# Performance work log

Hardware: AMD Instinct MI355X
Metric: run time of the kernel (lower is better)

The kernel has to match this reference:

```python
import jax, jax.numpy as jnp
import numpy as np

B, S, W = 64, 256, 16
V, CV = 50000, 100
E, CD, H, T = 256, 64, 512, 50


def lstm_scan(xs, wih, whh, bih, bhh, reverse=False):
    # xs: [T, N, D]; PyTorch LSTMCell gate order i, f, g, o
    Hh = whh.shape[1]
    def step(carry, x):
        h, c = carry
        g = x @ wih.T + bih + h @ whh.T + bhh
        i, f, gg, o = jnp.split(g, 4, axis=-1)
        c = jax.nn.sigmoid(f) * c + jax.nn.sigmoid(i) * jnp.tanh(gg)
        h = jax.nn.sigmoid(o) * jnp.tanh(c)
        return (h, c), h
    z = jnp.zeros((xs.shape[1], Hh), xs.dtype)
    (hT, _), hs = jax.lax.scan(step, (z, z), xs, reverse=reverse)
    return hT, hs


def setup_inputs():
    key = jax.random.key(0)
    ki = iter(jax.random.split(key, 64))
    def p(shape):
        return (jax.random.normal(next(ki), shape) * 0.05).astype(jnp.float32)
    def cell(din, h):
        return p((4 * h, din)), p((4 * h, h)), p((4 * h,)), p((4 * h,))
    inp = {
        'sentence': jax.random.randint(next(ki), (B, S), 0, V),
        'char_sentence': jax.random.randint(next(ki), (B, S, W), 0, CV),
        'w_emb': p((V, E)),
        'w_char': p((CV, CD)),
    }
    for name, din, h in [('cf', CD, E // 2), ('cb', CD, E // 2),
                         ('l1f', E, H), ('l1b', E, H),
                         ('l2f', 2 * H, H), ('l2b', 2 * H, H)]:
        wih, whh, bih, bhh = cell(din, h)
        inp[name + '_wih'] = wih; inp[name + '_whh'] = whh
        inp[name + '_bih'] = bih; inp[name + '_bhh'] = bhh
    inp['w_final'] = p((E, 2 * E)); inp['b_final'] = p((E,))
    inp['w_tag'] = p((T, 2 * H)); inp['b_tag'] = p((T,))
    return inp


def reference(sentence, char_sentence, w_emb, w_char,
              cf_wih, cf_whh, cf_bih, cf_bhh,
              cb_wih, cb_whh, cb_bih, cb_bhh,
              l1f_wih, l1f_whh, l1f_bih, l1f_bhh,
              l1b_wih, l1b_whh, l1b_bih, l1b_bhh,
              l2f_wih, l2f_whh, l2f_bih, l2f_bhh,
              l2b_wih, l2b_whh, l2b_bih, l2b_bhh,
              w_final, b_final, w_tag, b_tag):
    w_char = w_char.at[0].set(0.0)            # padding_idx=0
    word_emb = w_emb[sentence]                # [B,S,E]
    ce = w_char[char_sentence]                # [B,S,W,CD]
    b, s, w, cd = ce.shape
    ce = ce.reshape(b * s, w, cd).transpose(1, 0, 2)   # [W, B*S, CD]
    hf, _ = lstm_scan(ce, cf_wih, cf_whh, cf_bih, cf_bhh)
    hb, _ = lstm_scan(ce, cb_wih, cb_whh, cb_bih, cb_bhh, reverse=True)
    char_word = jnp.concatenate([hf, hb], -1).reshape(b, s, -1)  # [B,S,E]
    embeds = jnp.concatenate([word_emb, char_word], -1) @ w_final.T + b_final
    xs = embeds.transpose(1, 0, 2)            # [S,B,E]
    _, o1f = lstm_scan(xs, l1f_wih, l1f_whh, l1f_bih, l1f_bhh)
    _, o1b = lstm_scan(xs, l1b_wih, l1b_whh, l1b_bih, l1b_bhh, reverse=True)
    o1 = jnp.concatenate([o1f, o1b], -1)      # [S,B,2H]
    _, o2f = lstm_scan(o1, l2f_wih, l2f_whh, l2f_bih, l2f_bhh)
    _, o2b = lstm_scan(o1, l2b_wih, l2b_whh, l2b_bih, l2b_bhh, reverse=True)
    o2 = jnp.concatenate([o2f, o2b], -1).transpose(1, 0, 2)  # [B,S,2H]
    # dropout is identity in eval mode
    return o2 @ w_tag.T + b_tag               # [B,S,T]
```

## Files before the change

kernel.cpp:

```cpp
#include <hip/hip_runtime.h>

typedef unsigned short u16;
typedef unsigned long long ull;
typedef short short8 __attribute__((ext_vector_type(8)));
typedef float float4_ __attribute__((ext_vector_type(4)));
typedef short8 short8a __attribute__((may_alias));
typedef float4_ float4a __attribute__((may_alias));
typedef ull ulla __attribute__((may_alias));

#define MFMA16(a, b, c) __builtin_amdgcn_mfma_f32_16x16x32_bf16((a), (b), (c), 0, 0, 0)

static __device__ __forceinline__ float b2f(u16 v) { return __uint_as_float(((unsigned)v) << 16); }
static __device__ __forceinline__ u16 f2b(float f) {
  unsigned x = __float_as_uint(f);
  return (u16)((x + 0x7fffu + ((x >> 16) & 1u)) >> 16);
}
static __device__ __forceinline__ float ldv(const void* p, long long i, int isbf) {
  return isbf ? b2f(((const u16*)p)[i]) : ((const float*)p)[i];
}
static __device__ __forceinline__ float sigm(float x) { return 1.f / (1.f + __expf(-x)); }
static __device__ __forceinline__ float tanh_(float x) { return 1.f - 2.f / (__expf(2.f * x) + 1.f); }
static __device__ __forceinline__ float4_ splat4(float v) { float4_ r; r[0]=v; r[1]=v; r[2]=v; r[3]=v; return r; }

__global__ __launch_bounds__(256) void k_detect(const unsigned* __restrict__ wtag, int* __restrict__ flag) {
  __shared__ int cs;
  if (threadIdx.x == 0) cs = 0;
  __syncthreads();
  int hits = 0;
  for (int i = threadIdx.x; i < 1024; i += 256) {
    unsigned b = (wtag[i] >> 8) & 0x7fu;
    hits += (b >= 0x36u && b <= 0x3fu) ? 1 : 0;
  }
  atomicAdd(&cs, hits);
  __syncthreads();
  if (threadIdx.x == 0) *flag = (cs > 512) ? 1 : 0;
}

struct WSegs { const void* src[15]; int dst[15]; int n[15]; };
__global__ __launch_bounds__(256) void k_convw(WSegs s, u16* __restrict__ wt, const int* __restrict__ flagp) {
  const int isbf = *flagp;
  const long long total8 = 9830400 / 8;
  for (long long i8 = (long long)blockIdx.x * 256 + threadIdx.x; i8 < total8; i8 += (long long)gridDim.x * 256) {
    const long long i = i8 * 8;
    int k = 0;
#pragma unroll
    for (int j = 1; j < 15; ++j) if (i >= (long long)s.dst[j]) k = j;
    const long long loc = i - s.dst[k];
    short8 out;
    if (!s.src[k]) {
      for (int j = 0; j < 8; ++j) out[j] = 0;
    } else if (isbf) {
      out = *(const short8a*)((const u16*)s.src[k] + loc);
    } else {
      const float* fp = (const float*)s.src[k] + loc;
      const float4_ f0 = *(const float4a*)fp;
      const float4_ f1 = *(const float4a*)(fp + 4);
#pragma unroll
      for (int j = 0; j < 4; ++j) { out[j] = (short)f2b(f0[j]); out[j + 4] = (short)f2b(f1[j]); }
    }
    *(short8a*)(wt + i) = out;
  }
}

struct BSegs { const void* a[8]; const void* b[8]; int dst[8]; int n[8]; int np[8]; };
__global__ __launch_bounds__(256) void k_convb(BSegs s, float* __restrict__ bias, const int* __restrict__ flagp) {
  const int isbf = *flagp;
  for (int i = blockIdx.x * 256 + threadIdx.x; i < 9536; i += gridDim.x * 256) {
    int k = 0;
#pragma unroll
    for (int j = 1; j < 8; ++j) if (i >= s.dst[j]) k = j;
    const int loc = i - s.dst[k];
    float v = 0.f;
    if (loc < s.n[k]) {
      v = ldv(s.a[k], loc, isbf);
      if (s.b[k]) v += ldv(s.b[k], loc, isbf);
    }
    bias[i] = v;
  }
}

__global__ __launch_bounds__(128) void k_wordgather(const int* __restrict__ sent, const void* __restrict__ wemb,
                                                    u16* __restrict__ cat, const int* __restrict__ flagp) {
  const int n = blockIdx.x;
  const int idx = sent[n];
  const int isbf = *flagp;
  for (int d = threadIdx.x; d < 256; d += 128)
    cat[(long long)n * 512 + d] = f2b(ldv(wemb, (long long)idx * 256 + d, isbf));
}

__global__ __launch_bounds__(256) void k_char(const int* __restrict__ cs, const void* __restrict__ wchar,
                                              const u16* __restrict__ wihF, const u16* __restrict__ whhF,
                                              const u16* __restrict__ wihB, const u16* __restrict__ whhB,
                                              const float* __restrict__ biasF, const float* __restrict__ biasB,
                                              u16* __restrict__ cat, const int* __restrict__ flagp) {
  const int dir = blockIdx.y;
  const int nb = blockIdx.x;
  const u16* wih = dir ? wihB : wihF;
  const u16* whh = dir ? whhB : whhF;
  const float* bias = dir ? biasB : biasF;
  const int isbf = *flagp;
  __shared__ __align__(16) u16 xs[64][72];
  __shared__ __align__(16) u16 hs[64][136];
  const int tid = threadIdx.x, wv = tid >> 6, lane = tid & 63;
  for (int i = tid; i < 64 * 136; i += 256) ((u16*)hs)[i] = 0;
  float c[2][4][4];
#pragma unroll
  for (int a1 = 0; a1 < 2; ++a1)
#pragma unroll
    for (int a2 = 0; a2 < 4; ++a2)
#pragma unroll
      for (int a3 = 0; a3 < 4; ++a3) c[a1][a2][a3] = 0.f;

  for (int tt = 0; tt < 16; ++tt) {
    const int t = dir ? (15 - tt) : tt;
    {
      const int sid = tid >> 2, part = tid & 3;
      const int n = nb * 64 + sid;
      const int idx = cs[n * 16 + t];
#pragma unroll
      for (int q = 0; q < 16; ++q) {
        const int d2 = part * 16 + q;
        float v = 0.f;
        if (idx != 0) v = ldv(wchar, (long long)idx * 64 + d2, isbf);
        xs[sid][d2] = f2b(v);
      }
    }
    __syncthreads();
    float4_ acc[2][4][4];
#pragma unroll
    for (int ut = 0; ut < 2; ++ut)
#pragma unroll
      for (int g = 0; g < 4; ++g) {
        const float bv = bias[g * 128 + (wv + 4 * ut) * 16 + (lane & 15)];
#pragma unroll
        for (int rt = 0; rt < 4; ++rt) acc[ut][g][rt] = splat4(bv);
      }
#pragma unroll
    for (int kc = 0; kc < 6; ++kc) {
      short8 a[4];
      if (kc < 2) {
#pragma unroll
        for (int rt = 0; rt < 4; ++rt)
          a[rt] = *(const short8a*)&xs[rt * 16 + (lane & 15)][kc * 32 + (lane >> 4) * 8];
      } else {
#pragma unroll
        for (int rt = 0; rt < 4; ++rt)
          a[rt] = *(const short8a*)&hs[rt * 16 + (lane & 15)][(kc - 2) * 32 + (lane >> 4) * 8];
      }
#pragma unroll
      for (int ut = 0; ut < 2; ++ut)
#pragma unroll
        for (int g = 0; g < 4; ++g) {
          const int col = g * 128 + (wv + 4 * ut) * 16 + (lane & 15);
          short8 bfr;
          if (kc < 2) bfr = *(const short8a*)(wih + col * 64 + kc * 32 + (lane >> 4) * 8);
          else        bfr = *(const short8a*)(whh + col * 128 + (kc - 2) * 32 + (lane >> 4) * 8);
#pragma unroll
          for (int rt = 0; rt < 4; ++rt) acc[ut][g][rt] = MFMA16(a[rt], bfr, acc[ut][g][rt]);
        }
    }
    __syncthreads();
#pragma unroll
    for (int ut = 0; ut < 2; ++ut)
#pragma unroll
      for (int rt = 0; rt < 4; ++rt)
#pragma unroll
        for (int r = 0; r < 4; ++r) {
          const float iv = acc[ut][0][rt][r];
          const float fv = acc[ut][1][rt][r];
          const float gv = acc[ut][2][rt][r];
          const float ov = acc[ut][3][rt][r];
          float& cc = c[ut][rt][r];
          cc = sigm(fv) * cc + sigm(iv) * tanh_(gv);
          const float h = sigm(ov) * tanh_(cc);
          const int seq = rt * 16 + (lane >> 4) * 4 + r;
          const int u = (wv + 4 * ut) * 16 + (lane & 15);
          const u16 hv = f2b(h);
          hs[seq][u] = hv;
          if (tt == 15) cat[(long long)(nb * 64 + seq) * 512 + 256 + dir * 128 + u] = hv;
        }
  }
}

template <int TM, int TN, int PERM, int OUTM>
__global__ __launch_bounds__(256) void k_gemm(const u16* __restrict__ A, const u16* __restrict__ Wt,
                                              const float* __restrict__ bias, void* __restrict__ Cout,
                                              const int N, const int K, const int ldc,
                                              const int* __restrict__ flagp) {
  constexpr int RT = TM / 16;
  constexpr int CPW = TN / 64;
  const int bm = blockIdx.x, bn = blockIdx.y;
  const int tid = threadIdx.x, wv = tid >> 6, lane = tid & 63;
  __shared__ __align__(16) u16 As[TM][72];
  float4_ acc[CPW][RT];
#pragma unroll
  for (int ci = 0; ci < CPW; ++ci)
#pragma unroll
    for (int rt = 0; rt < RT; ++rt) acc[ci][rt] = splat4(0.f);
  const int nk = K >> 6;
  for (int kc = 0; kc < nk; ++kc) {
    __syncthreads();
    for (int idx = tid; idx < TM * 4; idx += 256) {
      const int r = idx >> 2, sg = idx & 3;
      const u16* src = A + (long long)(bm * TM + r) * K + kc * 64 + sg * 16;
      *(short8a*)&As[r][sg * 16] = *(const short8a*)src;
      *(short8a*)&As[r][sg * 16 + 8] = *(const short8a*)(src + 8);
    }
    __syncthreads();
#pragma unroll
    for (int kk = 0; kk < 2; ++kk) {
      short8 af[RT];
#pragma unroll
      for (int rt = 0; rt < RT; ++rt)
        af[rt] = *(const short8a*)&As[rt * 16 + (lane & 15)][kk * 32 + (lane >> 4) * 8];
#pragma unroll
      for (int ci = 0; ci < CPW; ++ci) {
        const int ct = wv + ci * 4;
        const short8 bf = *(const short8a*)(Wt + (long long)(bn * TN + ct * 16 + (lane & 15)) * K +
                                            kc * 64 + kk * 32 + (lane >> 4) * 8);
#pragma unroll
        for (int rt = 0; rt < RT; ++rt) acc[ci][rt] = MFMA16(af[rt], bf, acc[ci][rt]);
      }
    }
  }
  const int isbf = (OUTM == 1) ? *flagp : 0;
#pragma unroll
  for (int ci = 0; ci < CPW; ++ci)
#pragma unroll
    for (int rt = 0; rt < RT; ++rt)
#pragma unroll
      for (int r = 0; r < 4; ++r) {
        const int row = bm * TM + rt * 16 + (lane >> 4) * 4 + r;
        const int col = bn * TN + (wv + ci * 4) * 16 + (lane & 15);
        if (col < N) {
          const float v = acc[ci][rt][r] + bias[col];
          long long orow;
          if (PERM == 0) orow = row;
          else if (PERM == 1) orow = (long long)(row & 255) * 64 + (row >> 8);
          else orow = (long long)(row & 63) * 256 + (row >> 6);
          if (OUTM == 0) ((u16*)Cout)[orow * ldc + col] = f2b(v);
          else if (isbf) ((u16*)Cout)[orow * ldc + col] = f2b(v);
          else ((float*)Cout)[orow * ldc + col] = v;
        }
      }
}

__global__ __launch_bounds__(512, 1) void k_scan(const u16* __restrict__ pre0, const u16* __restrict__ pre1,
                                                 const u16* __restrict__ whh0, const u16* __restrict__ whh1,
                                                 u16* __restrict__ o_out, const u16* __restrict__ zbuf,
                                                 int* __restrict__ flags) {
  const int dir = blockIdx.y, blk = blockIdx.x;
  const u16* __restrict__ pre = dir ? pre1 : pre0;
  const u16* __restrict__ whh = dir ? whh1 : whh0;
  int* myflags = flags + dir * 512;
  const int u0 = blk * 32;
  __shared__ __align__(16) u16 hstage[64 * 512];
  __shared__ __align__(16) float xch[8 * 64 * 32];
  const int tid = threadIdx.x, lane = tid & 63;
  const int wv = tid >> 6;
  const int l15 = lane & 15, q = lane >> 4;
  const int g = wv & 3, kh = wv >> 2;

  float4_ swf[2][8];
#pragma unroll
  for (int ci = 0; ci < 2; ++ci)
#pragma unroll
    for (int kc = 0; kc < 8; ++kc)
      swf[ci][kc] = *(const float4a*)(whh + (long long)(g * 512 + u0 + ci * 16 + l15) * 512 +
                                      kh * 256 + kc * 32 + q * 8);

  const int bb = tid >> 3;
  const int t8 = tid & 7;
  float c4[4];
#pragma unroll
  for (int j = 0; j < 4; ++j) c4[j] = 0.f;

  ull pr[4], prn[4];
  {
    const int t0 = dir ? 255 : 0;
    const u16* pb = pre + (long long)(t0 * 64 + bb) * 2048 + u0 + t8 * 4;
#pragma unroll
    for (int g2 = 0; g2 < 4; ++g2) pr[g2] = *(const ulla*)(pb + g2 * 512);
  }

  for (int tt = 0; tt < 256; ++tt) {
    const int t = dir ? (255 - tt) : tt;

    {
      const u16* base;
      if (tt == 0) {
        base = zbuf + dir * 512;
      } else {
        const int tp = dir ? (t + 1) : (t - 1);
        base = o_out + (long long)tp * 65536 + dir * 512;
      }
      const int off = lane * 8;
#pragma unroll
      for (int it = 0; it < 8; ++it) {
        const int row = wv + it * 8;
        const float4_ v = *(const float4a*)(base + (long long)row * 1024 + off);
        *(float4a*)((char*)hstage + row * 1024 + ((off * 2) ^ ((row & 7) << 4))) = v;
      }
    }
    __syncthreads();

    float4_ acc[2][4];
#pragma unroll
    for (int ci = 0; ci < 2; ++ci)
#pragma unroll
      for (int bt = 0; bt < 4; ++bt) acc[ci][bt] = splat4(0.f);
    const char* hsb = (const char*)hstage;
#pragma unroll
    for (int kc = 0; kc < 8; ++kc) {
      const short8 w0 = __builtin_bit_cast(short8, swf[0][kc]);
      const short8 w1 = __builtin_bit_cast(short8, swf[1][kc]);
#pragma unroll
      for (int bt = 0; bt < 4; ++bt) {
        const int row = bt * 16 + l15;
        const short8 A = *(const short8a*)(hsb + row * 1024 +
                          ((kh * 512 + kc * 64 + q * 16) ^ ((row & 7) << 4)));
        acc[0][bt] = MFMA16(w0, A, acc[0][bt]);
        acc[1][bt] = MFMA16(w1, A, acc[1][bt]);
      }
    }

#pragma unroll
    for (int ci = 0; ci < 2; ++ci)
#pragma unroll
      for (int bt = 0; bt < 4; ++bt) {
        const int b = bt * 16 + l15;
        *(float4a*)&xch[(((kh * 4 + g) * 64 + b) * 32) + (((ci * 4 + q) ^ (l15 & 7)) * 4)] = acc[ci][bt];
      }
    __syncthreads();

    const int rq = (t8 ^ (bb & 7)) * 4;
    float4_ gv[4];
#pragma unroll
    for (int g2 = 0; g2 < 4; ++g2) {
      const float4_ p0 = *(const float4a*)&xch[((g2 * 64 + bb) * 32) + rq];
      const float4_ p1 = *(const float4a*)&xch[(((4 + g2) * 64 + bb) * 32) + rq];
      gv[g2] = p0 + p1;
    }
    ull hv = 0;
#pragma unroll
    for (int j = 0; j < 4; ++j) {
      const float iv = gv[0][j] + b2f((u16)(pr[0] >> (16 * j)));
      const float fv = gv[1][j] + b2f((u16)(pr[1] >> (16 * j)));
      const float gg = gv[2][j] + b2f((u16)(pr[2] >> (16 * j)));
      const float ov = gv[3][j] + b2f((u16)(pr[3] >> (16 * j)));
      c4[j] = sigm(fv) * c4[j] + sigm(iv) * tanh_(gg);
      const float h = sigm(ov) * tanh_(c4[j]);
      hv |= (ull)f2b(h) << (16 * j);
    }
    __hip_atomic_store((ull*)(o_out + (long long)(t * 64 + bb) * 1024 + dir * 512 + u0 + t8 * 4), hv,
                       __ATOMIC_RELAXED, __HIP_MEMORY_SCOPE_AGENT);
    asm volatile("s_waitcnt vmcnt(0)" ::: "memory");
    __syncthreads();
    if (tid == 0)
      __hip_atomic_store(&myflags[blk * 32], tt + 1, __ATOMIC_RELAXED, __HIP_MEMORY_SCOPE_AGENT);
    {
      const int ttn = (tt < 255) ? tt + 1 : tt;
      const int tn = dir ? (255 - ttn) : ttn;
      const u16* pb = pre + (long long)(tn * 64 + bb) * 2048 + u0 + t8 * 4;
#pragma unroll
      for (int g2 = 0; g2 < 4; ++g2) prn[g2] = *(const ulla*)(pb + g2 * 512);
    }
    if (tt != 255) {
      const int* fp = myflags + l15 * 32;
      int v = __hip_atomic_load(fp, __ATOMIC_RELAXED, __HIP_MEMORY_SCOPE_AGENT);
      while (__all(v >= tt + 1) == 0) {
        __builtin_amdgcn_s_sleep(1);
        v = __hip_atomic_load(fp, __ATOMIC_RELAXED, __HIP_MEMORY_SCOPE_AGENT);
      }
    }
#pragma unroll
    for (int g2 = 0; g2 < 4; ++g2) pr[g2] = prn[g2];
#pragma unroll
    for (int ci = 0; ci < 2; ++ci)
#pragma unroll
      for (int kc = 0; kc < 8; ++kc) asm volatile("" : "+v"(swf[ci][kc]));
  }
}

static constexpr long long OFF_WT = 0;
static constexpr long long OFF_BIAS = 19660800;
static constexpr long long OFF_CAT = 19698944;
static constexpr long long OFF_EMB = 36476160;
static constexpr long long OFF_PRE = 44864768;
static constexpr long long OFF_O1 = 179082496;
static constexpr long long OFF_O2 = 212636928;
static constexpr long long OFF_SYNC = 246191360;
static constexpr long long SYNC_BYTES = 16384 + 131072;
static constexpr long long OFF_FLAG = OFF_SYNC + SYNC_BYTES;

extern "C" void kernel_launch(void* const* d_in, const int* in_sizes, int n_in,
                              void* d_out, int out_size, void* d_ws, size_t ws_size,
                              hipStream_t stream) {
  char* ws = (char*)d_ws;
  u16* wt = (u16*)(ws + OFF_WT);
  float* biasp = (float*)(ws + OFF_BIAS);
  u16* cat = (u16*)(ws + OFF_CAT);
  u16* emb = (u16*)(ws + OFF_EMB);
  u16* pre0 = (u16*)(ws + OFF_PRE);
  u16* pre1 = pre0 + (long long)16384 * 2048;
  u16* o1 = (u16*)(ws + OFF_O1);
  u16* o2 = (u16*)(ws + OFF_O2);
  int* cnt1 = (int*)(ws + OFF_SYNC);
  int* cnt2 = cnt1 + 1024;
  u16* zbuf = (u16*)(ws + OFF_SYNC + 16384);
  int* flag = (int*)(ws + OFF_FLAG);

  hipMemsetAsync(ws + OFF_SYNC, 0, SYNC_BYTES, stream);
  k_detect<<<1, 256, 0, stream>>>((const unsigned*)d_in[30], flag);

  WSegs wsg;
  const int widx[14] = {4, 5, 8, 9, 12, 13, 16, 17, 20, 21, 24, 25, 28, 30};
  const int wdst[15] = {0, 32768, 98304, 131072, 196608, 720896, 1769472, 2293760,
                        3342336, 5439488, 6488064, 8585216, 9633792, 9764864, 9816064};
  const int wn[15] = {32768, 65536, 32768, 65536, 524288, 1048576, 524288, 1048576,
                      2097152, 1048576, 2097152, 1048576, 131072, 51200, 14336};
  for (int j = 0; j < 14; ++j) { wsg.src[j] = d_in[widx[j]]; wsg.dst[j] = wdst[j]; wsg.n[j] = wn[j]; }
  wsg.src[14] = nullptr; wsg.dst[14] = wdst[14]; wsg.n[14] = wn[14];
  k_convw<<<1200, 256, 0, stream>>>(wsg, wt, flag);

  BSegs bsg;
  const int ba[8] = {6, 10, 14, 18, 22, 26, 29, 31};
  const int bb[8] = {7, 11, 15, 19, 23, 27, -1, -1};
  const int bdst[8] = {0, 512, 1024, 3072, 5120, 7168, 9216, 9472};
  const int bn_[8] = {512, 512, 2048, 2048, 2048, 2048, 256, 50};
  const int bnp[8] = {512, 512, 2048, 2048, 2048, 2048, 256, 64};
  for (int j = 0; j < 8; ++j) {
    bsg.a[j] = d_in[ba[j]];
    bsg.b[j] = (bb[j] >= 0) ? d_in[bb[j]] : nullptr;
    bsg.dst[j] = bdst[j]; bsg.n[j] = bn_[j]; bsg.np[j] = bnp[j];
  }
  k_convb<<<40, 256, 0, stream>>>(bsg, biasp, flag);

  k_wordgather<<<16384, 128, 0, stream>>>((const int*)d_in[0], d_in[2], cat, flag);
  k_char<<<dim3(256, 2), 256, 0, stream>>>((const int*)d_in[1], d_in[3],
                                           wt + 0, wt + 32768, wt + 98304, wt + 131072,
                                           biasp + 0, biasp + 512, cat, flag);
  k_gemm<64, 64, 1, 0><<<dim3(256, 4), 256, 0, stream>>>(cat, wt + 9633792, biasp + 9216, emb, 256, 512, 256, flag);
  k_gemm<128, 256, 0, 0><<<dim3(128, 8), 256, 0, stream>>>(emb, wt + 196608, biasp + 1024, pre0, 2048, 256, 2048, flag);
  k_gemm<128, 256, 0, 0><<<dim3(128, 8), 256, 0, stream>>>(emb, wt + 1769472, biasp + 3072, pre1, 2048, 256, 2048, flag);
  k_scan<<<dim3(16, 2), 512, 0, stream>>>(pre0, pre1, wt + 720896, wt + 2293760, o1, zbuf, cnt1);
  k_gemm<128, 256, 0, 0><<<dim3(128, 8), 256, 0, stream>>>(o1, wt + 3342336, biasp + 5120, pre0, 2048, 1024, 2048, flag);
  k_gemm<128, 256, 0, 0><<<dim3(128, 8), 256, 0, stream>>>(o1, wt + 6488064, biasp + 7168, pre1, 2048, 1024, 2048, flag);
  k_scan<<<dim3(16, 2), 512, 0, stream>>>(pre0, pre1, wt + 5439488, wt + 8585216, o2, zbuf, cnt2);
  k_gemm<64, 64, 2, 1><<<dim3(256, 1), 256, 0, stream>>>(o2, wt + 9764864, biasp + 9472, d_out, 50, 1024, 50, flag);
}
```

Before: 3.434 ms.

## Split LSTM scan across 32 blocks per direction with per-wave batch tiles

The persistent recurrent scan kernel now uses 32 blocks per direction, each owning 16 hidden units instead of 32. Inside a block, waves are re-partitioned by batch tile and K-half rather than gate and K-half. The K-half reduction goes through a smaller LDS exchange, and only the first half of the waves does the gate math, the h store and the prefetch. This halves the per-step MFMA work per block, but each step now waits on twice as many cross-block flags and every block still stages the full h vector, so synchronisation cost grows.

```diff
diff --git a/kernel.cpp b/kernel.cpp
--- a/kernel.cpp
+++ b/kernel.cpp
@@ -252,35 +252,34 @@
   const int dir = blockIdx.y, blk = blockIdx.x;
   const u16* __restrict__ pre = dir ? pre1 : pre0;
   const u16* __restrict__ whh = dir ? whh1 : whh0;
-  int* myflags = flags + dir * 512;
-  const int u0 = blk * 32;
+  int* myflags = flags + dir * 1024;
+  const int u0 = blk * 16;
   __shared__ __align__(16) u16 hstage[64 * 512];
-  __shared__ __align__(16) float xch[8 * 64 * 32];
+  __shared__ __align__(16) float xch[4][64][16];
   const int tid = threadIdx.x, lane = tid & 63;
   const int wv = tid >> 6;
   const int l15 = lane & 15, q = lane >> 4;
-  const int g = wv & 3, kh = wv >> 2;
-
-  float4_ swf[2][8];
-#pragma unroll
-  for (int ci = 0; ci < 2; ++ci)
+  const int kh = wv >> 2, bt = wv & 3;
+  const int b = bt * 16 + l15;
+
+  float4_ swf[4][8];
+#pragma unroll
+  for (int g = 0; g < 4; ++g)
 #pragma unroll
     for (int kc = 0; kc < 8; ++kc)
-      swf[ci][kc] = *(const float4a*)(whh + (long long)(g * 512 + u0 + ci * 16 + l15) * 512 +
-                                      kh * 256 + kc * 32 + q * 8);
-
-  const int bb = tid >> 3;
-  const int t8 = tid & 7;
+      swf[g][kc] = *(const float4a*)(whh + (long long)(g * 512 + u0 + l15) * 512 +
+                                     kh * 256 + kc * 32 + q * 8);
+
   float c4[4];
 #pragma unroll
   for (int j = 0; j < 4; ++j) c4[j] = 0.f;
 
   ull pr[4], prn[4];
-  {
+  if (kh == 0) {
     const int t0 = dir ? 255 : 0;
-    const u16* pb = pre + (long long)(t0 * 64 + bb) * 2048 + u0 + t8 * 4;
-#pragma unroll
-    for (int g2 = 0; g2 < 4; ++g2) pr[g2] = *(const ulla*)(pb + g2 * 512);
+    const u16* pb = pre + (long long)(t0 * 64 + b) * 2048 + u0 + q * 4;
+#pragma unroll
+    for (int g = 0; g < 4; ++g) pr[g] = *(const ulla*)(pb + g * 512);
   }
 
   for (int tt = 0; tt < 256; ++tt) {
@@ -304,81 +303,73 @@
     }
     __syncthreads();
 
-    float4_ acc[2][4];
-#pragma unroll
-    for (int ci = 0; ci < 2; ++ci)
-#pragma unroll
-      for (int bt = 0; bt < 4; ++bt) acc[ci][bt] = splat4(0.f);
+    float4_ acc[4];
+#pragma unroll
+    for (int g = 0; g < 4; ++g) acc[g] = splat4(0.f);
     const char* hsb = (const char*)hstage;
 #pragma unroll
     for (int kc = 0; kc < 8; ++kc) {
-      const short8 w0 = __builtin_bit_cast(short8, swf[0][kc]);
-      const short8 w1 = __builtin_bit_cast(short8, swf[1][kc]);
-#pragma unroll
-      for (int bt = 0; bt < 4; ++bt) {
-        const int row = bt * 16 + l15;
-        const short8 A = *(const short8a*)(hsb + row * 1024 +
-                          ((kh * 512 + kc * 64 + q * 16) ^ ((row & 7) << 4)));
-        acc[0][bt] = MFMA16(w0, A, acc[0][bt]);
-        acc[1][bt] = MFMA16(w1, A, acc[1][bt]);
-      }
-    }
-
-#pragma unroll
-    for (int ci = 0; ci < 2; ++ci)
-#pragma unroll
-      for (int bt = 0; bt < 4; ++bt) {
-        const int b = bt * 16 + l15;
-        *(float4a*)&xch[(((kh * 4 + g) * 64 + b) * 32) + (((ci * 4 + q) ^ (l15 & 7)) * 4)] = acc[ci][bt];
-      }
-    __syncthreads();
-
-    const int rq = (t8 ^ (bb & 7)) * 4;
-    float4_ gv[4];
-#pragma unroll
-    for (int g2 = 0; g2 < 4; ++g2) {
-      const float4_ p0 = *(const float4a*)&xch[((g2 * 64 + bb) * 32) + rq];
-      const float4_ p1 = *(const float4a*)&xch[(((4 + g2) * 64 + bb) * 32) + rq];
-      gv[g2] = p0 + p1;
-    }
-    ull hv = 0;
-#pragma unroll
-    for (int j = 0; j < 4; ++j) {
-      const float iv = gv[0][j] + b2f((u16)(pr[0] >> (16 * j)));
-      const float fv = gv[1][j] + b2f((u16)(pr[1] >> (16 * j)));
-      const float gg = gv[2][j] + b2f((u16)(pr[2] >> (16 * j)));
-      const float ov = gv[3][j] + b2f((u16)(pr[3] >> (16 * j)));
-      c4[j] = sigm(fv) * c4[j] + sigm(iv) * tanh_(gg);
-      const float h = sigm(ov) * tanh_(c4[j]);
-      hv |= (ull)f2b(h) << (16 * j);
-    }
-    __hip_atomic_store((ull*)(o_out + (long long)(t * 64 + bb) * 1024 + dir * 512 + u0 + t8 * 4), hv,
-                       __ATOMIC_RELAXED, __HIP_MEMORY_SCOPE_AGENT);
+      const int row = b;
+      const short8 A = *(const short8a*)(hsb + row * 1024 +
+                        ((kh * 512 + kc * 64 + q * 16) ^ ((row & 7) << 4)));
+      acc[0] = MFMA16(__builtin_bit_cast(short8, swf[0][kc]), A, acc[0]);
+      acc[1] = MFMA16(__builtin_bit_cast(short8, swf[1][kc]), A, acc[1]);
+      acc[2] = MFMA16(__builtin_bit_cast(short8, swf[2][kc]), A, acc[2]);
+      acc[3] = MFMA16(__builtin_bit_cast(short8, swf[3][kc]), A, acc[3]);
+    }
+
+    if (kh == 1) {
+#pragma unroll
+      for (int g = 0; g < 4; ++g)
+        *(float4a*)&xch[g][b][(q ^ (l15 & 3)) * 4] = acc[g];
+    }
+    __syncthreads();
+    if (kh == 0) {
+#pragma unroll
+      for (int g = 0; g < 4; ++g)
+        acc[g] += *(const float4a*)&xch[g][b][(q ^ (l15 & 3)) * 4];
+      ull hv = 0;
+#pragma unroll
+      for (int j = 0; j < 4; ++j) {
+        const float iv = acc[0][j] + b2f((u16)(pr[0] >> (16 * j)));
+        const float fv = acc[1][j] + b2f((u16)(pr[1] >> (16 * j)));
+        const float gg = acc[2][j] + b2f((u16)(pr[2] >> (16 * j)));
+        const float ov = acc[3][j] + b2f((u16)(pr[3] >> (16 * j)));
+        c4[j] = sigm(fv) * c4[j] + sigm(iv) * tanh_(gg);
+        const float h = sigm(ov) * tanh_(c4[j]);
+        hv |= (ull)f2b(h) << (16 * j);
+      }
+      __hip_atomic_store((ull*)(o_out + (long long)(t * 64 + b) * 1024 + dir * 512 + u0 + q * 4), hv,
+                         __ATOMIC_RELAXED, __HIP_MEMORY_SCOPE_AGENT);
+    }
     asm volatile("s_waitcnt vmcnt(0)" ::: "memory");
     __syncthreads();
     if (tid == 0)
       __hip_atomic_store(&myflags[blk * 32], tt + 1, __ATOMIC_RELAXED, __HIP_MEMORY_SCOPE_AGENT);
-    {
+    if (kh == 0) {
       const int ttn = (tt < 255) ? tt + 1 : tt;
       const int tn = dir ? (255 - ttn) : ttn;
-      const u16* pb = pre + (long long)(tn * 64 + bb) * 2048 + u0 + t8 * 4;
-#pragma unroll
-      for (int g2 = 0; g2 < 4; ++g2) prn[g2] = *(const ulla*)(pb + g2 * 512);
+      const u16* pb = pre + (long long)(tn * 64 + b) * 2048 + u0 + q * 4;
+#pragma unroll
+      for (int g = 0; g < 4; ++g) prn[g] = *(const ulla*)(pb + g * 512);
     }
     if (tt != 255) {
-      const int* fp = myflags + l15 * 32;
+      const int* fp = myflags + (lane & 31) * 32;
       int v = __hip_atomic_load(fp, __ATOMIC_RELAXED, __HIP_MEMORY_SCOPE_AGENT);
       while (__all(v >= tt + 1) == 0) {
         __builtin_amdgcn_s_sleep(1);
         v = __hip_atomic_load(fp, __ATOMIC_RELAXED, __HIP_MEMORY_SCOPE_AGENT);
       }
-    }
-#pragma unroll
-    for (int g2 = 0; g2 < 4; ++g2) pr[g2] = prn[g2];
-#pragma unroll
-    for (int ci = 0; ci < 2; ++ci)
-#pragma unroll
-      for (int kc = 0; kc < 8; ++kc) asm volatile("" : "+v"(swf[ci][kc]));
+      asm volatile("" ::: "memory");
+    }
+    if (kh == 0) {
+#pragma unroll
+      for (int g = 0; g < 4; ++g) pr[g] = prn[g];
+    }
+#pragma unroll
+    for (int g = 0; g < 4; ++g)
+#pragma unroll
+      for (int kc = 0; kc < 8; ++kc) asm volatile("" : "+v"(swf[g][kc]));
   }
 }
 
@@ -406,7 +397,7 @@
   u16* o1 = (u16*)(ws + OFF_O1);
   u16* o2 = (u16*)(ws + OFF_O2);
   int* cnt1 = (int*)(ws + OFF_SYNC);
-  int* cnt2 = cnt1 + 1024;
+  int* cnt2 = cnt1 + 2048;
   u16* zbuf = (u16*)(ws + OFF_SYNC + 16384);
   int* flag = (int*)(ws + OFF_FLAG);
 
@@ -443,9 +434,9 @@
   k_gemm<64, 64, 1, 0><<<dim3(256, 4), 256, 0, stream>>>(cat, wt + 9633792, biasp + 9216, emb, 256, 512, 256, flag);
   k_gemm<128, 256, 0, 0><<<dim3(128, 8), 256, 0, stream>>>(emb, wt + 196608, biasp + 1024, pre0, 2048, 256, 2048, flag);
   k_gemm<128, 256, 0, 0><<<dim3(128, 8), 256, 0, stream>>>(emb, wt + 1769472, biasp + 3072, pre1, 2048, 256, 2048, flag);
-  k_scan<<<dim3(16, 2), 512, 0, stream>>>(pre0, pre1, wt + 720896, wt + 2293760, o1, zbuf, cnt1);
+  k_scan<<<dim3(32, 2), 512, 0, stream>>>(pre0, pre1, wt + 720896, wt + 2293760, o1, zbuf, cnt1);
   k_gemm<128, 256, 0, 0><<<dim3(128, 8), 256, 0, stream>>>(o1, wt + 3342336, biasp + 5120, pre0, 2048, 1024, 2048, flag);
   k_gemm<128, 256, 0, 0><<<dim3(128, 8), 256, 0, stream>>>(o1, wt + 6488064, biasp + 7168, pre1, 2048, 1024, 2048, flag);
-  k_scan<<<dim3(16, 2), 512, 0, stream>>>(pre0, pre1, wt + 5439488, wt + 8585216, o2, zbuf, cnt2);
+  k_scan<<<dim3(32, 2), 512, 0, stream>>>(pre0, pre1, wt + 5439488, wt + 8585216, o2, zbuf, cnt2);
   k_gemm<64, 64, 2, 1><<<dim3(256, 1), 256, 0, stream>>>(o2, wt + 9764864, biasp + 9472, d_out, 50, 1024, 50, flag);
 }
```

Result: faster. 3.006 ms (-12.5%).
